# Optimization experiments

Measured on AMD Instinct MI355X. Metric: run time of the kernel, lower is better.

## Reference

```python
import jax, jax.numpy as jnp
import numpy as np

N = 8192      # nodes
E = 262144    # edges (avg degree 32)
D_IN = 128    # feat dim (out_channels)
D_H = 256     # hidden_channels * 2
D_OUT = 64    # in_channels (final embedding dim)


def _sage_pool(feat, src, dst, n, Wp, bp, Ws, Wn, b, ew):
    # DGL SAGEConv('pool'): h_pool = relu(fc_pool(feat)); msg = h_pool[src] * ew;
    # h_neigh = max over in-edges (0 for isolated nodes);
    # out = fc_self(feat) + fc_neigh(h_neigh) + bias
    h = jax.nn.relu(feat @ Wp + bp)                          # [N, d_in]
    msg = h[src] * ew[:, None]                               # [E, d_in]
    agg = jax.ops.segment_max(msg, dst, num_segments=n)      # [N, d_in], -inf if no in-edges
    agg = jnp.where(jnp.isfinite(agg), agg, 0.0)
    return feat @ Ws + agg @ Wn + b


def setup_inputs() -> dict:
    key = jax.random.key(0)
    ks = jax.random.split(key, 20)
    feat = jax.random.normal(ks[0], (N, D_IN), dtype=jnp.float32)
    src = jax.random.randint(ks[1], (E,), 0, N)
    dst = jax.random.randint(ks[2], (E,), 0, N)
    edge_weight = jax.random.uniform(ks[3], (E,), dtype=jnp.float32)

    def lin(k, din, dout):
        return jax.random.normal(k, (din, dout), dtype=jnp.float32) / np.float32(np.sqrt(din))

    params = {}
    dims = [(D_IN, D_H), (D_H, D_H), (D_H, D_OUT)]
    i = 4
    for l, (di, do) in enumerate(dims, 1):
        params[f"Wp{l}"] = lin(ks[i], di, di); i += 1
        params[f"bp{l}"] = jnp.zeros((di,), jnp.float32)
        params[f"Ws{l}"] = lin(ks[i], di, do); i += 1
        params[f"Wn{l}"] = lin(ks[i], di, do); i += 1
        params[f"b{l}"] = jnp.zeros((do,), jnp.float32)

    return dict(feat=feat, src=src, dst=dst, edge_weight=edge_weight, n_nodes=N, **params)


def reference(feat, src, dst, edge_weight, n_nodes,
              Wp1, bp1, Ws1, Wn1, b1,
              Wp2, bp2, Ws2, Wn2, b2,
              Wp3, bp3, Ws3, Wn3, b3):
    hd = jax.nn.relu(_sage_pool(feat, src, dst, n_nodes, Wp1, bp1, Ws1, Wn1, b1, edge_weight))
    hd = jax.nn.relu(_sage_pool(hd,   src, dst, n_nodes, Wp2, bp2, Ws2, Wn2, b2, edge_weight))
    hd = jax.nn.relu(_sage_pool(hd,   src, dst, n_nodes, Wp3, bp3, Ws3, Wn3, b3, edge_weight))
    adj_rec = hd @ hd.T                                      # [N, N]
    return hd, adj_rec
```

## Files before the change

### kernel.cpp

```cpp
#include <hip/hip_runtime.h>
#include <hip/hip_bf16.h>

#define NN 8192
#define NE 262144
#define CAP 96

typedef __attribute__((ext_vector_type(8))) __bf16 bf16x8;
typedef __attribute__((ext_vector_type(4))) float f32x4;

__device__ __forceinline__ ushort f2b(float v) {
    __hip_bfloat16 b = __float2bfloat16(v);
    return *reinterpret_cast<ushort*>(&b);
}
__device__ __forceinline__ uint pack2(float lo, float hi) {
    return (uint)f2b(lo) | ((uint)f2b(hi) << 16);
}
__device__ __forceinline__ float b2f(ushort u) {
    return __uint_as_float(((uint)u) << 16);
}

struct PrepArgs {
    const int* src; const int* dst; const float* ew;
    int* cnt; uint2* slots;
    const float* w[9]; ushort* wt[9];
};

__global__ __launch_bounds__(256) void prep_scatter_k(PrepArgs a) {
    const int bid = blockIdx.x, tid = threadIdx.x;
    if (bid < 1024) {
        int e = bid * 256 + tid;
        int d = a.dst[e];
        int p = atomicAdd(&a.cnt[d], 1);
        if (p < CAP) a.slots[(size_t)d * CAP + p] = make_uint2((uint)a.src[e], __float_as_uint(a.ew[e]));
        return;
    }
    int id = (bid - 1024) * 256 + tid;
    if (id >= 376832) return;
    const int cum[10] = {0, 16384, 49152, 81920, 147456, 212992, 278528, 344064, 360448, 376832};
    const int KK[9] = {128, 128, 128, 256, 256, 256, 256, 256, 256};
    const int LN[9] = {7, 8, 8, 8, 8, 8, 8, 6, 6};
    int m = 0;
#pragma unroll
    for (int t = 1; t < 9; ++t) m += (id >= cum[t]);
    int local = id - cum[m];
    int K = KK[m], ln = LN[m];
    int k = local >> ln, n = local & ((1 << ln) - 1);
    a.wt[m][n * K + k] = f2b(a.w[m][local]);
}

#define AWK 136

template <int BM, int BN, bool A1F32, bool RELU, int OUTMODE, bool ADDC>
__global__ __launch_bounds__(256, 4) void gemm_k(
    const void* __restrict__ Av, const ushort* __restrict__ BT, int K,
    const float* __restrict__ bias, const ushort* __restrict__ cin,
    float* __restrict__ Cf, ushort* __restrict__ Cb, int N) {
    constexpr int MI = BM / 32, NJ = BN / 32;
    __shared__ __align__(16) ushort As[BM * AWK];
    __shared__ __align__(16) ushort Bs[BN * AWK];

    const int tid = threadIdx.x, lane = tid & 63, wave = tid >> 6;
    const int wm = (wave >> 1) * (BM / 2), wn = (wave & 1) * (BN / 2);
    const int r16 = lane & 15, kb = lane >> 4;
    const int m0 = blockIdx.y * BM, n0 = blockIdx.x * BN;

    f32x4 acc[MI][NJ];
#pragma unroll
    for (int i = 0; i < MI; ++i)
#pragma unroll
        for (int j = 0; j < NJ; ++j) acc[i][j] = (f32x4)(0.f);

    for (int k0 = 0; k0 < K; k0 += 128) {
        if constexpr (A1F32) {
            const float* A = (const float*)Av;
#pragma unroll
            for (int rep = 0; rep < BM / 8; ++rep) {
                int id = rep * 256 + tid;
                int row = id >> 5, c = id & 31;
                float4 f = *(const float4*)&A[(size_t)(m0 + row) * K + k0 + c * 4];
                uint2 o; o.x = pack2(f.x, f.y); o.y = pack2(f.z, f.w);
                *(uint2*)&As[row * AWK + c * 4] = o;
            }
        } else {
            const ushort* A = (const ushort*)Av;
#pragma unroll
            for (int rep = 0; rep < BM / 16; ++rep) {
                int id = rep * 256 + tid;
                int row = id >> 4, c = id & 15;
                *(bf16x8*)&As[row * AWK + c * 8] =
                    *(const bf16x8*)&A[(size_t)(m0 + row) * K + k0 + c * 8];
            }
        }
#pragma unroll
        for (int rep = 0; rep < BN / 16; ++rep) {
            int id = rep * 256 + tid;
            int row = id >> 4, c = id & 15;
            *(bf16x8*)&Bs[row * AWK + c * 8] =
                *(const bf16x8*)&BT[(size_t)(n0 + row) * K + k0 + c * 8];
        }
        __syncthreads();
#pragma unroll
        for (int kc = 0; kc < 4; ++kc) {
            bf16x8 a[MI], b[NJ];
#pragma unroll
            for (int i = 0; i < MI; ++i)
                a[i] = *(const bf16x8*)&As[(wm + 16 * i + r16) * AWK + kc * 32 + kb * 8];
#pragma unroll
            for (int j = 0; j < NJ; ++j)
                b[j] = *(const bf16x8*)&Bs[(wn + 16 * j + r16) * AWK + kc * 32 + kb * 8];
#pragma unroll
            for (int i = 0; i < MI; ++i)
#pragma unroll
                for (int j = 0; j < NJ; ++j)
                    acc[i][j] = __builtin_amdgcn_mfma_f32_16x16x32_bf16(a[i], b[j], acc[i][j], 0, 0, 0);
        }
        __syncthreads();
    }

#pragma unroll
    for (int i = 0; i < MI; ++i) {
#pragma unroll
        for (int j = 0; j < NJ; ++j) {
            int col = n0 + wn + 16 * j + r16;
            float bv = ADDC ? 0.f : bias[col];
#pragma unroll
            for (int r = 0; r < 4; ++r) {
                int row = m0 + wm + 16 * i + kb * 4 + r;
                float v = acc[i][j][r];
                if constexpr (ADDC) v += b2f(cin[(size_t)row * N + col]);
                else v += bv;
                if (RELU) v = fmaxf(v, 0.f);
                if (OUTMODE != 0) Cf[(size_t)row * N + col] = v;
                if (OUTMODE != 1) Cb[(size_t)row * N + col] = f2b(v);
            }
        }
    }
}

template <int DIN, int DOUT, bool A1F32>
__global__ __launch_bounds__(256, 4) void seg_self_k(
    const ushort* __restrict__ Pin, const int* __restrict__ cnt,
    const uint2* __restrict__ slots, ushort* __restrict__ G,
    const void* __restrict__ Av, const ushort* __restrict__ WsT,
    const float* __restrict__ bias, ushort* __restrict__ Cself) {
    constexpr int BM = (DOUT == 64) ? 32 : 64;
    constexpr int NBX = DOUT / 64;
    constexpr int MI = BM / 32, NJ = 2;
    __shared__ __align__(16) ushort As[BM * AWK];
    __shared__ __align__(16) ushort Bs[64 * AWK];

    const int tid = threadIdx.x, lane = tid & 63, wave = tid >> 6;

    if (blockIdx.x < 2048) {
        constexpr int FPL = DIN / 64;
        int node = blockIdx.x * 4 + wave;
        int f0 = lane * FPL;
        int n = cnt[node]; if (n > CAP) n = CAP;
        const uint2* sl = &slots[(size_t)node * CAP];
        float mx[FPL];
#pragma unroll
        for (int i = 0; i < FPL; ++i) mx[i] = 0.f;
        auto upd = [&](uint s, float w) {
            const uint* hp = (const uint*)&Pin[(size_t)s * DIN + f0];
#pragma unroll
            for (int c = 0; c < FPL / 2; ++c) {
                uint u = hp[c];
                float lo = __uint_as_float(u << 16);
                float hi = __uint_as_float(u & 0xffff0000u);
                mx[2 * c] = fmaxf(mx[2 * c], lo * w);
                mx[2 * c + 1] = fmaxf(mx[2 * c + 1], hi * w);
            }
        };
        int e = 0;
        for (; e + 8 <= n; e += 8) {
            uint2 d[8];
#pragma unroll
            for (int t = 0; t < 8; ++t) d[t] = sl[e + t];
#pragma unroll
            for (int t = 0; t < 8; ++t) upd(d[t].x, __uint_as_float(d[t].y));
        }
        for (; e < n; ++e) { uint2 d = sl[e]; upd(d.x, __uint_as_float(d.y)); }
        uint* gp = (uint*)&G[(size_t)node * DIN + f0];
#pragma unroll
        for (int c = 0; c < FPL / 2; ++c) gp[c] = pack2(mx[2 * c], mx[2 * c + 1]);
        return;
    }

    const int bx = blockIdx.x - 2048;
    const int n0 = (bx % NBX) * 64, m0 = (bx / NBX) * BM;
    const int wm = (wave >> 1) * (BM / 2), wn = (wave & 1) * 32;
    const int r16 = lane & 15, kb = lane >> 4;

    f32x4 acc[MI][NJ];
#pragma unroll
    for (int i = 0; i < MI; ++i)
#pragma unroll
        for (int j = 0; j < NJ; ++j) acc[i][j] = (f32x4)(0.f);

    for (int k0 = 0; k0 < DIN; k0 += 128) {
        if constexpr (A1F32) {
            const float* A = (const float*)Av;
#pragma unroll
            for (int rep = 0; rep < BM / 8; ++rep) {
                int id = rep * 256 + tid;
                int row = id >> 5, c = id & 31;
                float4 f = *(const float4*)&A[(size_t)(m0 + row) * DIN + k0 + c * 4];
                uint2 o; o.x = pack2(f.x, f.y); o.y = pack2(f.z, f.w);
                *(uint2*)&As[row * AWK + c * 4] = o;
            }
        } else {
            const ushort* A = (const ushort*)Av;
#pragma unroll
            for (int rep = 0; rep < BM / 16; ++rep) {
                int id = rep * 256 + tid;
                int row = id >> 4, c = id & 15;
                *(bf16x8*)&As[row * AWK + c * 8] =
                    *(const bf16x8*)&A[(size_t)(m0 + row) * DIN + k0 + c * 8];
            }
        }
#pragma unroll
        for (int rep = 0; rep < 4; ++rep) {
            int id = rep * 256 + tid;
            int row = id >> 4, c = id & 15;
            *(bf16x8*)&Bs[row * AWK + c * 8] =
                *(const bf16x8*)&WsT[(size_t)(n0 + row) * DIN + k0 + c * 8];
        }
        __syncthreads();
#pragma unroll
        for (int kc = 0; kc < 4; ++kc) {
            bf16x8 a[MI], b[NJ];
#pragma unroll
            for (int i = 0; i < MI; ++i)
                a[i] = *(const bf16x8*)&As[(wm + 16 * i + r16) * AWK + kc * 32 + kb * 8];
#pragma unroll
            for (int j = 0; j < NJ; ++j)
                b[j] = *(const bf16x8*)&Bs[(wn + 16 * j + r16) * AWK + kc * 32 + kb * 8];
#pragma unroll
            for (int i = 0; i < MI; ++i)
#pragma unroll
                for (int j = 0; j < NJ; ++j)
                    acc[i][j] = __builtin_amdgcn_mfma_f32_16x16x32_bf16(a[i], b[j], acc[i][j], 0, 0, 0);
        }
        __syncthreads();
    }

#pragma unroll
    for (int i = 0; i < MI; ++i) {
#pragma unroll
        for (int j = 0; j < NJ; ++j) {
            int col = n0 + wn + 16 * j + r16;
            float bv = bias[col];
#pragma unroll
            for (int r = 0; r < 4; ++r) {
                int row = m0 + wm + 16 * i + kb * 4 + r;
                Cself[(size_t)row * DOUT + col] = f2b(acc[i][j][r] + bv);
            }
        }
    }
}

__global__ __launch_bounds__(256) void aat_k(const ushort* __restrict__ H,
                                             float* __restrict__ C) {
    __shared__ __align__(16) ushort As[128 * 72];
    __shared__ __align__(16) ushort Bs[128 * 72];
    int tid = threadIdx.x, lane = tid & 63, wave = tid >> 6;
    int wm = (wave >> 1) * 64, wn = (wave & 1) * 64;
    int r16 = lane & 15, kb = lane >> 4;
    int m0 = blockIdx.y * 128, n0 = blockIdx.x * 128;

#pragma unroll
    for (int rep = 0; rep < 4; ++rep) {
        int id = rep * 256 + tid;
        int row = id >> 3, c = id & 7;
        *(bf16x8*)&As[row * 72 + c * 8] = *(const bf16x8*)&H[(size_t)(m0 + row) * 64 + c * 8];
        *(bf16x8*)&Bs[row * 72 + c * 8] = *(const bf16x8*)&H[(size_t)(n0 + row) * 64 + c * 8];
    }
    __syncthreads();

    f32x4 acc[4][4];
#pragma unroll
    for (int i = 0; i < 4; ++i)
#pragma unroll
        for (int j = 0; j < 4; ++j) acc[i][j] = (f32x4)(0.f);

#pragma unroll
    for (int kc = 0; kc < 2; ++kc) {
        bf16x8 a[4], b[4];
#pragma unroll
        for (int i = 0; i < 4; ++i)
            a[i] = *(const bf16x8*)&As[(wm + 16 * i + r16) * 72 + kc * 32 + kb * 8];
#pragma unroll
        for (int j = 0; j < 4; ++j)
            b[j] = *(const bf16x8*)&Bs[(wn + 16 * j + r16) * 72 + kc * 32 + kb * 8];
#pragma unroll
        for (int i = 0; i < 4; ++i)
#pragma unroll
            for (int j = 0; j < 4; ++j)
                acc[i][j] = __builtin_amdgcn_mfma_f32_16x16x32_bf16(a[i], b[j], acc[i][j], 0, 0, 0);
    }

#pragma unroll
    for (int i = 0; i < 4; ++i) {
#pragma unroll
        for (int j = 0; j < 4; ++j) {
            int col = n0 + wn + 16 * j + r16;
#pragma unroll
            for (int r = 0; r < 4; ++r) {
                size_t row = m0 + wm + 16 * i + kb * 4 + r;
                C[row * NN + col] = acc[i][j][r];
            }
        }
    }
}

extern "C" void kernel_launch(void* const* d_in, const int* in_sizes, int n_in,
                              void* d_out, int out_size, void* d_ws, size_t ws_size,
                              hipStream_t stream) {
    const float* feat = (const float*)d_in[0];
    const int* src = (const int*)d_in[1];
    const int* dst = (const int*)d_in[2];
    const float* ew = (const float*)d_in[3];
    const float* Wp1 = (const float*)d_in[5];
    const float* bp1 = (const float*)d_in[6];
    const float* Ws1 = (const float*)d_in[7];
    const float* Wn1 = (const float*)d_in[8];
    const float* b1  = (const float*)d_in[9];
    const float* Wp2 = (const float*)d_in[10];
    const float* bp2 = (const float*)d_in[11];
    const float* Ws2 = (const float*)d_in[12];
    const float* Wn2 = (const float*)d_in[13];
    const float* b2  = (const float*)d_in[14];
    const float* Wp3 = (const float*)d_in[15];
    const float* bp3 = (const float*)d_in[16];
    const float* Ws3 = (const float*)d_in[17];
    const float* Wn3 = (const float*)d_in[18];
    const float* b3  = (const float*)d_in[19];

    float* out = (float*)d_out;
    float* adj = out + (size_t)NN * 64;

    char* ws = (char*)d_ws;
    int* cnt      = (int*)(ws + 0x0);
    uint2* slots  = (uint2*)(ws + 0x10000);
    ushort* Wp1T = (ushort*)(ws + 0x620000);
    ushort* Ws1T = (ushort*)(ws + 0x628000);
    ushort* Wn1T = (ushort*)(ws + 0x638000);
    ushort* Wp2T = (ushort*)(ws + 0x648000);
    ushort* Ws2T = (ushort*)(ws + 0x668000);
    ushort* Wn2T = (ushort*)(ws + 0x688000);
    ushort* Wp3T = (ushort*)(ws + 0x6A8000);
    ushort* Ws3T = (ushort*)(ws + 0x6C8000);
    ushort* Wn3T = (ushort*)(ws + 0x6D0000);
    ushort* P  = (ushort*)(ws + 0x700000);
    ushort* G  = (ushort*)(ws + 0xB00000);
    ushort* X  = (ushort*)(ws + 0xF00000);
    ushort* Y  = (ushort*)(ws + 0x1300000);
    ushort* Cs = (ushort*)(ws + 0x1700000);
    ushort* hdb = (ushort*)(ws + 0x1B00000);

    hipMemsetAsync(cnt, 0, NN * sizeof(int), stream);

    PrepArgs pa;
    pa.src = src; pa.dst = dst; pa.ew = ew; pa.cnt = cnt; pa.slots = slots;
    const float* wsrc[9] = {Wp1, Ws1, Wn1, Wp2, Ws2, Wn2, Wp3, Ws3, Wn3};
    ushort* wdst[9] = {Wp1T, Ws1T, Wn1T, Wp2T, Ws2T, Wn2T, Wp3T, Ws3T, Wn3T};
    for (int i = 0; i < 9; ++i) { pa.w[i] = wsrc[i]; pa.wt[i] = wdst[i]; }
    prep_scatter_k<<<1024 + 1472, 256, 0, stream>>>(pa);

    gemm_k<64, 64, true, true, 0, false><<<dim3(2, 128), 256, 0, stream>>>(
        feat, Wp1T, 128, bp1, nullptr, nullptr, P, 128);
    seg_self_k<128, 256, true><<<2048 + 512, 256, 0, stream>>>(
        P, cnt, slots, G, feat, Ws1T, b1, Cs);
    gemm_k<64, 64, false, true, 0, true><<<dim3(4, 128), 256, 0, stream>>>(
        G, Wn1T, 128, nullptr, Cs, nullptr, X, 256);

    gemm_k<64, 64, false, true, 0, false><<<dim3(4, 128), 256, 0, stream>>>(
        X, Wp2T, 256, bp2, nullptr, nullptr, P, 256);
    seg_self_k<256, 256, false><<<2048 + 512, 256, 0, stream>>>(
        P, cnt, slots, G, X, Ws2T, b2, Cs);
    gemm_k<64, 64, false, true, 0, true><<<dim3(4, 128), 256, 0, stream>>>(
        G, Wn2T, 256, nullptr, Cs, nullptr, Y, 256);

    gemm_k<64, 64, false, true, 0, false><<<dim3(4, 128), 256, 0, stream>>>(
        Y, Wp3T, 256, bp3, nullptr, nullptr, P, 256);
    seg_self_k<256, 64, false><<<2048 + 256, 256, 0, stream>>>(
        P, cnt, slots, G, Y, Ws3T, b3, Cs);
    gemm_k<32, 64, false, true, 2, true><<<dim3(1, 256), 256, 0, stream>>>(
        G, Wn3T, 256, nullptr, Cs, out, hdb, 64);

    aat_k<<<dim3(NN / 128, NN / 128), 256, 0, stream>>>(hdb, adj);
}
```

Before: 165.3 us.

## Fuse pool and self projections into one GEMM, split segment-max kernel

Measured after the change: 187.1 us. +13.2%, slower.

```diff
diff --git a/kernel.cpp b/kernel.cpp
--- a/kernel.cpp
+++ b/kernel.cpp
@@ -4,6 +4,7 @@
 #define NN 8192
 #define NE 262144
 #define CAP 96
+#define AWK 136
 
 typedef __attribute__((ext_vector_type(8))) __bf16 bf16x8;
 typedef __attribute__((ext_vector_type(4))) float f32x4;
@@ -23,6 +24,9 @@
     const int* src; const int* dst; const float* ew;
     int* cnt; uint2* slots;
     const float* w[9]; ushort* wt[9];
+    const float* bp1; const float* b1; const float* bp2; const float* b2;
+    const float* bp3; const float* b3;
+    float* bcat1; float* bcat2; float* bcat3;
 };
 
 __global__ __launch_bounds__(256) void prep_scatter_k(PrepArgs a) {
@@ -34,6 +38,17 @@
         if (p < CAP) a.slots[(size_t)d * CAP + p] = make_uint2((uint)a.src[e], __float_as_uint(a.ew[e]));
         return;
     }
+    if (bid == 2496) {
+        for (int i = tid; i < 128; i += 256) a.bcat1[i] = a.bp1[i];
+        for (int i = tid; i < 256; i += 256) {
+            a.bcat1[128 + i] = a.b1[i];
+            a.bcat2[i] = a.bp2[i];
+            a.bcat2[256 + i] = a.b2[i];
+            a.bcat3[i] = a.bp3[i];
+        }
+        for (int i = tid; i < 64; i += 256) a.bcat3[256 + i] = a.b3[i];
+        return;
+    }
     int id = (bid - 1024) * 256 + tid;
     if (id >= 376832) return;
     const int cum[10] = {0, 16384, 49152, 81920, 147456, 212992, 278528, 344064, 360448, 376832};
@@ -48,33 +63,29 @@
     a.wt[m][n * K + k] = f2b(a.w[m][local]);
 }
 
-#define AWK 136
-
-template <int BM, int BN, bool A1F32, bool RELU, int OUTMODE, bool ADDC>
-__global__ __launch_bounds__(256, 4) void gemm_k(
-    const void* __restrict__ Av, const ushort* __restrict__ BT, int K,
-    const float* __restrict__ bias, const ushort* __restrict__ cin,
-    float* __restrict__ Cf, ushort* __restrict__ Cb, int N) {
-    constexpr int MI = BM / 32, NJ = BN / 32;
-    __shared__ __align__(16) ushort As[BM * AWK];
-    __shared__ __align__(16) ushort Bs[BN * AWK];
+template <int NP, int NS, bool A1F32>
+__global__ __launch_bounds__(256, 4) void ps_gemm_k(
+    const void* __restrict__ Av, const ushort* __restrict__ WT, int K,
+    const float* __restrict__ bcat, ushort* __restrict__ P, ushort* __restrict__ Cs) {
+    __shared__ __align__(16) ushort As[64 * AWK];
+    __shared__ __align__(16) ushort Bs[64 * AWK];
 
     const int tid = threadIdx.x, lane = tid & 63, wave = tid >> 6;
-    const int wm = (wave >> 1) * (BM / 2), wn = (wave & 1) * (BN / 2);
+    const int wm = (wave >> 1) * 32, wn = (wave & 1) * 32;
     const int r16 = lane & 15, kb = lane >> 4;
-    const int m0 = blockIdx.y * BM, n0 = blockIdx.x * BN;
-
-    f32x4 acc[MI][NJ];
-#pragma unroll
-    for (int i = 0; i < MI; ++i)
-#pragma unroll
-        for (int j = 0; j < NJ; ++j) acc[i][j] = (f32x4)(0.f);
+    const int m0 = blockIdx.y * 64, n0 = blockIdx.x * 64;
+
+    f32x4 acc[2][2];
+#pragma unroll
+    for (int i = 0; i < 2; ++i)
+#pragma unroll
+        for (int j = 0; j < 2; ++j) acc[i][j] = (f32x4)(0.f);
 
     for (int k0 = 0; k0 < K; k0 += 128) {
         if constexpr (A1F32) {
             const float* A = (const float*)Av;
 #pragma unroll
-            for (int rep = 0; rep < BM / 8; ++rep) {
+            for (int rep = 0; rep < 8; ++rep) {
                 int id = rep * 256 + tid;
                 int row = id >> 5, c = id & 31;
                 float4 f = *(const float4*)&A[(size_t)(m0 + row) * K + k0 + c * 4];
@@ -84,7 +95,7 @@
         } else {
             const ushort* A = (const ushort*)Av;
 #pragma unroll
-            for (int rep = 0; rep < BM / 16; ++rep) {
+            for (int rep = 0; rep < 4; ++rep) {
                 int id = rep * 256 + tid;
                 int row = id >> 4, c = id & 15;
                 *(bf16x8*)&As[row * AWK + c * 8] =
@@ -92,153 +103,101 @@
             }
         }
 #pragma unroll
-        for (int rep = 0; rep < BN / 16; ++rep) {
-            int id = rep * 256 + tid;
-            int row = id >> 4, c = id & 15;
-            *(bf16x8*)&Bs[row * AWK + c * 8] =
-                *(const bf16x8*)&BT[(size_t)(n0 + row) * K + k0 + c * 8];
-        }
-        __syncthreads();
-#pragma unroll
-        for (int kc = 0; kc < 4; ++kc) {
-            bf16x8 a[MI], b[NJ];
-#pragma unroll
-            for (int i = 0; i < MI; ++i)
-                a[i] = *(const bf16x8*)&As[(wm + 16 * i + r16) * AWK + kc * 32 + kb * 8];
-#pragma unroll
-            for (int j = 0; j < NJ; ++j)
-                b[j] = *(const bf16x8*)&Bs[(wn + 16 * j + r16) * AWK + kc * 32 + kb * 8];
-#pragma unroll
-            for (int i = 0; i < MI; ++i)
-#pragma unroll
-                for (int j = 0; j < NJ; ++j)
-                    acc[i][j] = __builtin_amdgcn_mfma_f32_16x16x32_bf16(a[i], b[j], acc[i][j], 0, 0, 0);
-        }
-        __syncthreads();
-    }
-
-#pragma unroll
-    for (int i = 0; i < MI; ++i) {
-#pragma unroll
-        for (int j = 0; j < NJ; ++j) {
-            int col = n0 + wn + 16 * j + r16;
-            float bv = ADDC ? 0.f : bias[col];
-#pragma unroll
-            for (int r = 0; r < 4; ++r) {
-                int row = m0 + wm + 16 * i + kb * 4 + r;
-                float v = acc[i][j][r];
-                if constexpr (ADDC) v += b2f(cin[(size_t)row * N + col]);
-                else v += bv;
-                if (RELU) v = fmaxf(v, 0.f);
-                if (OUTMODE != 0) Cf[(size_t)row * N + col] = v;
-                if (OUTMODE != 1) Cb[(size_t)row * N + col] = f2b(v);
-            }
-        }
-    }
-}
-
-template <int DIN, int DOUT, bool A1F32>
-__global__ __launch_bounds__(256, 4) void seg_self_k(
-    const ushort* __restrict__ Pin, const int* __restrict__ cnt,
-    const uint2* __restrict__ slots, ushort* __restrict__ G,
-    const void* __restrict__ Av, const ushort* __restrict__ WsT,
-    const float* __restrict__ bias, ushort* __restrict__ Cself) {
-    constexpr int BM = (DOUT == 64) ? 32 : 64;
-    constexpr int NBX = DOUT / 64;
-    constexpr int MI = BM / 32, NJ = 2;
-    __shared__ __align__(16) ushort As[BM * AWK];
-    __shared__ __align__(16) ushort Bs[64 * AWK];
-
-    const int tid = threadIdx.x, lane = tid & 63, wave = tid >> 6;
-
-    if (blockIdx.x < 2048) {
-        constexpr int FPL = DIN / 64;
-        int node = blockIdx.x * 4 + wave;
-        int f0 = lane * FPL;
-        int n = cnt[node]; if (n > CAP) n = CAP;
-        const uint2* sl = &slots[(size_t)node * CAP];
-        float mx[FPL];
-#pragma unroll
-        for (int i = 0; i < FPL; ++i) mx[i] = 0.f;
-        auto upd = [&](uint s, float w) {
-            const uint* hp = (const uint*)&Pin[(size_t)s * DIN + f0];
-#pragma unroll
-            for (int c = 0; c < FPL / 2; ++c) {
-                uint u = hp[c];
-                float lo = __uint_as_float(u << 16);
-                float hi = __uint_as_float(u & 0xffff0000u);
-                mx[2 * c] = fmaxf(mx[2 * c], lo * w);
-                mx[2 * c + 1] = fmaxf(mx[2 * c + 1], hi * w);
-            }
-        };
-        int e = 0;
-        for (; e + 8 <= n; e += 8) {
-            uint2 d[8];
-#pragma unroll
-            for (int t = 0; t < 8; ++t) d[t] = sl[e + t];
-#pragma unroll
-            for (int t = 0; t < 8; ++t) upd(d[t].x, __uint_as_float(d[t].y));
-        }
-        for (; e < n; ++e) { uint2 d = sl[e]; upd(d.x, __uint_as_float(d.y)); }
-        uint* gp = (uint*)&G[(size_t)node * DIN + f0];
-#pragma unroll
-        for (int c = 0; c < FPL / 2; ++c) gp[c] = pack2(mx[2 * c], mx[2 * c + 1]);
-        return;
-    }
-
-    const int bx = blockIdx.x - 2048;
-    const int n0 = (bx % NBX) * 64, m0 = (bx / NBX) * BM;
-    const int wm = (wave >> 1) * (BM / 2), wn = (wave & 1) * 32;
-    const int r16 = lane & 15, kb = lane >> 4;
-
-    f32x4 acc[MI][NJ];
-#pragma unroll
-    for (int i = 0; i < MI; ++i)
-#pragma unroll
-        for (int j = 0; j < NJ; ++j) acc[i][j] = (f32x4)(0.f);
-
-    for (int k0 = 0; k0 < DIN; k0 += 128) {
-        if constexpr (A1F32) {
-            const float* A = (const float*)Av;
-#pragma unroll
-            for (int rep = 0; rep < BM / 8; ++rep) {
-                int id = rep * 256 + tid;
-                int row = id >> 5, c = id & 31;
-                float4 f = *(const float4*)&A[(size_t)(m0 + row) * DIN + k0 + c * 4];
-                uint2 o; o.x = pack2(f.x, f.y); o.y = pack2(f.z, f.w);
-                *(uint2*)&As[row * AWK + c * 4] = o;
-            }
-        } else {
-            const ushort* A = (const ushort*)Av;
-#pragma unroll
-            for (int rep = 0; rep < BM / 16; ++rep) {
-                int id = rep * 256 + tid;
-                int row = id >> 4, c = id & 15;
-                *(bf16x8*)&As[row * AWK + c * 8] =
-                    *(const bf16x8*)&A[(size_t)(m0 + row) * DIN + k0 + c * 8];
-            }
-        }
-#pragma unroll
         for (int rep = 0; rep < 4; ++rep) {
             int id = rep * 256 + tid;
             int row = id >> 4, c = id & 15;
             *(bf16x8*)&Bs[row * AWK + c * 8] =
-                *(const bf16x8*)&WsT[(size_t)(n0 + row) * DIN + k0 + c * 8];
+                *(const bf16x8*)&WT[(size_t)(n0 + row) * K + k0 + c * 8];
         }
         __syncthreads();
 #pragma unroll
         for (int kc = 0; kc < 4; ++kc) {
-            bf16x8 a[MI], b[NJ];
+            bf16x8 a[2], b[2];
+#pragma unroll
+            for (int i = 0; i < 2; ++i)
+                a[i] = *(const bf16x8*)&As[(wm + 16 * i + r16) * AWK + kc * 32 + kb * 8];
+#pragma unroll
+            for (int j = 0; j < 2; ++j)
+                b[j] = *(const bf16x8*)&Bs[(wn + 16 * j + r16) * AWK + kc * 32 + kb * 8];
+#pragma unroll
+            for (int i = 0; i < 2; ++i)
+#pragma unroll
+                for (int j = 0; j < 2; ++j)
+                    acc[i][j] = __builtin_amdgcn_mfma_f32_16x16x32_bf16(a[i], b[j], acc[i][j], 0, 0, 0);
+        }
+        __syncthreads();
+    }
+
+    const bool toP = (n0 < NP);
+    ushort* Co = toP ? P : Cs;
+    const int Nout = toP ? NP : NS;
+    const int nb = toP ? n0 : (n0 - NP);
+#pragma unroll
+    for (int i = 0; i < 2; ++i) {
+#pragma unroll
+        for (int j = 0; j < 2; ++j) {
+            int cl = wn + 16 * j + r16;
+            float bv = bcat[n0 + cl];
+#pragma unroll
+            for (int r = 0; r < 4; ++r) {
+                int row = m0 + wm + 16 * i + kb * 4 + r;
+                float v = acc[i][j][r] + bv;
+                if (toP) v = fmaxf(v, 0.f);
+                Co[(size_t)row * Nout + nb + cl] = f2b(v);
+            }
+        }
+    }
+}
+
+template <int BM, bool OUTF>
+__global__ __launch_bounds__(256, 4) void neigh_gemm_k(
+    const ushort* __restrict__ G, const ushort* __restrict__ WnT, int K,
+    const ushort* __restrict__ Cs, float* __restrict__ Cf,
+    ushort* __restrict__ Cb, int N) {
+    constexpr int MI = BM / 32;
+    __shared__ __align__(16) ushort As[BM * AWK];
+    __shared__ __align__(16) ushort Bs[64 * AWK];
+
+    const int tid = threadIdx.x, lane = tid & 63, wave = tid >> 6;
+    const int wm = (wave >> 1) * (BM / 2), wn = (wave & 1) * 32;
+    const int r16 = lane & 15, kb = lane >> 4;
+    const int m0 = blockIdx.y * BM, n0 = blockIdx.x * 64;
+
+    f32x4 acc[MI][2];
+#pragma unroll
+    for (int i = 0; i < MI; ++i)
+#pragma unroll
+        for (int j = 0; j < 2; ++j) acc[i][j] = (f32x4)(0.f);
+
+    for (int k0 = 0; k0 < K; k0 += 128) {
+#pragma unroll
+        for (int rep = 0; rep < BM / 16; ++rep) {
+            int id = rep * 256 + tid;
+            int row = id >> 4, c = id & 15;
+            *(bf16x8*)&As[row * AWK + c * 8] =
+                *(const bf16x8*)&G[(size_t)(m0 + row) * K + k0 + c * 8];
+        }
+#pragma unroll
+        for (int rep = 0; rep < 4; ++rep) {
+            int id = rep * 256 + tid;
+            int row = id >> 4, c = id & 15;
+            *(bf16x8*)&Bs[row * AWK + c * 8] =
+                *(const bf16x8*)&WnT[(size_t)(n0 + row) * K + k0 + c * 8];
+        }
+        __syncthreads();
+#pragma unroll
+        for (int kc = 0; kc < 4; ++kc) {
+            bf16x8 a[MI], b[2];
 #pragma unroll
             for (int i = 0; i < MI; ++i)
                 a[i] = *(const bf16x8*)&As[(wm + 16 * i + r16) * AWK + kc * 32 + kb * 8];
 #pragma unroll
-            for (int j = 0; j < NJ; ++j)
+            for (int j = 0; j < 2; ++j)
                 b[j] = *(const bf16x8*)&Bs[(wn + 16 * j + r16) * AWK + kc * 32 + kb * 8];
 #pragma unroll
             for (int i = 0; i < MI; ++i)
 #pragma unroll
-                for (int j = 0; j < NJ; ++j)
+                for (int j = 0; j < 2; ++j)
                     acc[i][j] = __builtin_amdgcn_mfma_f32_16x16x32_bf16(a[i], b[j], acc[i][j], 0, 0, 0);
         }
         __syncthreads();
@@ -247,16 +206,56 @@
 #pragma unroll
     for (int i = 0; i < MI; ++i) {
 #pragma unroll
-        for (int j = 0; j < NJ; ++j) {
+        for (int j = 0; j < 2; ++j) {
             int col = n0 + wn + 16 * j + r16;
-            float bv = bias[col];
 #pragma unroll
             for (int r = 0; r < 4; ++r) {
                 int row = m0 + wm + 16 * i + kb * 4 + r;
-                Cself[(size_t)row * DOUT + col] = f2b(acc[i][j][r] + bv);
-            }
-        }
-    }
+                float v = acc[i][j][r] + b2f(Cs[(size_t)row * N + col]);
+                v = fmaxf(v, 0.f);
+                if constexpr (OUTF) Cf[(size_t)row * N + col] = v;
+                Cb[(size_t)row * N + col] = f2b(v);
+            }
+        }
+    }
+}
+
+template <int DIN>
+__global__ __launch_bounds__(256) void seg_k(
+    const ushort* __restrict__ Pin, const int* __restrict__ cnt,
+    const uint2* __restrict__ slots, ushort* __restrict__ G) {
+    constexpr int FPL = DIN / 64;
+    const int lane = threadIdx.x & 63, wave = threadIdx.x >> 6;
+    int node = blockIdx.x * 4 + wave;
+    int f0 = lane * FPL;
+    int n = cnt[node]; if (n > CAP) n = CAP;
+    const uint2* sl = &slots[(size_t)node * CAP];
+    float mx[FPL];
+#pragma unroll
+    for (int i = 0; i < FPL; ++i) mx[i] = 0.f;
+    auto upd = [&](uint s, float w) {
+        const uint* hp = (const uint*)&Pin[(size_t)s * DIN + f0];
+#pragma unroll
+        for (int c = 0; c < FPL / 2; ++c) {
+            uint u = hp[c];
+            float lo = __uint_as_float(u << 16);
+            float hi = __uint_as_float(u & 0xffff0000u);
+            mx[2 * c] = fmaxf(mx[2 * c], lo * w);
+            mx[2 * c + 1] = fmaxf(mx[2 * c + 1], hi * w);
+        }
+    };
+    int e = 0;
+    for (; e + 8 <= n; e += 8) {
+        uint2 d[8];
+#pragma unroll
+        for (int t = 0; t < 8; ++t) d[t] = sl[e + t];
+#pragma unroll
+        for (int t = 0; t < 8; ++t) upd(d[t].x, __uint_as_float(d[t].y));
+    }
+    for (; e < n; ++e) { uint2 d = sl[e]; upd(d.x, __uint_as_float(d.y)); }
+    uint* gp = (uint*)&G[(size_t)node * DIN + f0];
+#pragma unroll
+    for (int c = 0; c < FPL / 2; ++c) gp[c] = pack2(mx[2 * c], mx[2 * c + 1]);
 }
 
 __global__ __launch_bounds__(256) void aat_k(const ushort* __restrict__ H,
@@ -307,7 +306,7 @@
 #pragma unroll
             for (int r = 0; r < 4; ++r) {
                 size_t row = m0 + wm + 16 * i + kb * 4 + r;
-                C[row * NN + col] = acc[i][j][r];
+                __builtin_nontemporal_store(acc[i][j][r], &C[row * NN + col]);
             }
         }
     }
@@ -342,15 +341,15 @@
     char* ws = (char*)d_ws;
     int* cnt      = (int*)(ws + 0x0);
     uint2* slots  = (uint2*)(ws + 0x10000);
-    ushort* Wp1T = (ushort*)(ws + 0x620000);
-    ushort* Ws1T = (ushort*)(ws + 0x628000);
-    ushort* Wn1T = (ushort*)(ws + 0x638000);
-    ushort* Wp2T = (ushort*)(ws + 0x648000);
-    ushort* Ws2T = (ushort*)(ws + 0x668000);
-    ushort* Wn2T = (ushort*)(ws + 0x688000);
-    ushort* Wp3T = (ushort*)(ws + 0x6A8000);
-    ushort* Ws3T = (ushort*)(ws + 0x6C8000);
-    ushort* Wn3T = (ushort*)(ws + 0x6D0000);
+    ushort* WpsT1 = (ushort*)(ws + 0x620000);
+    ushort* WpsT2 = (ushort*)(ws + 0x638000);
+    ushort* WpsT3 = (ushort*)(ws + 0x678000);
+    ushort* WnT1  = (ushort*)(ws + 0x6A0000);
+    ushort* WnT2  = (ushort*)(ws + 0x6B0000);
+    ushort* WnT3  = (ushort*)(ws + 0x6D0000);
+    float* bcat1  = (float*)(ws + 0x6D8000);
+    float* bcat2  = (float*)(ws + 0x6D9000);
+    float* bcat3  = (float*)(ws + 0x6DB000);
     ushort* P  = (ushort*)(ws + 0x700000);
     ushort* G  = (ushort*)(ws + 0xB00000);
     ushort* X  = (ushort*)(ws + 0xF00000);
@@ -363,30 +362,31 @@
     PrepArgs pa;
     pa.src = src; pa.dst = dst; pa.ew = ew; pa.cnt = cnt; pa.slots = slots;
     const float* wsrc[9] = {Wp1, Ws1, Wn1, Wp2, Ws2, Wn2, Wp3, Ws3, Wn3};
-    ushort* wdst[9] = {Wp1T, Ws1T, Wn1T, Wp2T, Ws2T, Wn2T, Wp3T, Ws3T, Wn3T};
+    ushort* wdst[9] = {WpsT1, WpsT1 + 128 * 128, WnT1,
+                       WpsT2, WpsT2 + 256 * 256, WnT2,
+                       WpsT3, WpsT3 + 256 * 256, WnT3};
     for (int i = 0; i < 9; ++i) { pa.w[i] = wsrc[i]; pa.wt[i] = wdst[i]; }
-    prep_scatter_k<<<1024 + 1472, 256, 0, stream>>>(pa);
-
-    gemm_k<64, 64, true, true, 0, false><<<dim3(2, 128), 256, 0, stream>>>(
-        feat, Wp1T, 128, bp1, nullptr, nullptr, P, 128);
-    seg_self_k<128, 256, true><<<2048 + 512, 256, 0, stream>>>(
-        P, cnt, slots, G, feat, Ws1T, b1, Cs);
-    gemm_k<64, 64, false, true, 0, true><<<dim3(4, 128), 256, 0, stream>>>(
-        G, Wn1T, 128, nullptr, Cs, nullptr, X, 256);
-
-    gemm_k<64, 64, false, true, 0, false><<<dim3(4, 128), 256, 0, stream>>>(
-        X, Wp2T, 256, bp2, nullptr, nullptr, P, 256);
-    seg_self_k<256, 256, false><<<2048 + 512, 256, 0, stream>>>(
-        P, cnt, slots, G, X, Ws2T, b2, Cs);
-    gemm_k<64, 64, false, true, 0, true><<<dim3(4, 128), 256, 0, stream>>>(
-        G, Wn2T, 256, nullptr, Cs, nullptr, Y, 256);
-
-    gemm_k<64, 64, false, true, 0, false><<<dim3(4, 128), 256, 0, stream>>>(
-        Y, Wp3T, 256, bp3, nullptr, nullptr, P, 256);
-    seg_self_k<256, 64, false><<<2048 + 256, 256, 0, stream>>>(
-        P, cnt, slots, G, Y, Ws3T, b3, Cs);
-    gemm_k<32, 64, false, true, 2, true><<<dim3(1, 256), 256, 0, stream>>>(
-        G, Wn3T, 256, nullptr, Cs, out, hdb, 64);
+    pa.bp1 = bp1; pa.b1 = b1; pa.bp2 = bp2; pa.b2 = b2; pa.bp3 = bp3; pa.b3 = b3;
+    pa.bcat1 = bcat1; pa.bcat2 = bcat2; pa.bcat3 = bcat3;
+    prep_scatter_k<<<2497, 256, 0, stream>>>(pa);
+
+    ps_gemm_k<128, 256, true><<<dim3(6, 128), 256, 0, stream>>>(
+        feat, WpsT1, 128, bcat1, P, Cs);
+    seg_k<128><<<NN / 4, 256, 0, stream>>>(P, cnt, slots, G);
+    neigh_gemm_k<64, false><<<dim3(4, 128), 256, 0, stream>>>(
+        G, WnT1, 128, Cs, nullptr, X, 256);
+
+    ps_gemm_k<256, 256, false><<<dim3(8, 128), 256, 0, stream>>>(
+        X, WpsT2, 256, bcat2, P, Cs);
+    seg_k<256><<<NN / 4, 256, 0, stream>>>(P, cnt, slots, G);
+    neigh_gemm_k<64, false><<<dim3(4, 128), 256, 0, stream>>>(
+        G, WnT2, 256, Cs, nullptr, Y, 256);
+
+    ps_gemm_k<256, 64, false><<<dim3(5, 128), 256, 0, stream>>>(
+        Y, WpsT3, 256, bcat3, P, Cs);
+    seg_k<256><<<NN / 4, 256, 0, stream>>>(P, cnt, slots, G);
+    neigh_gemm_k<32, true><<<dim3(1, 256), 256, 0, stream>>>(
+        G, WnT3, 256, Cs, out, hdb, 64);
 
     aat_k<<<dim3(NN / 128, NN / 128), 256, 0, stream>>>(hdb, adj);
 }
```

## Fuse edge scatter with layer-1 pool GEMM and interleave segment/GEMM blocks

Applied to the files above, without the earlier changes.

After: 163.0 us, median of 2. No clear change (-1.4%).

```diff
diff --git a/kernel.cpp b/kernel.cpp
--- a/kernel.cpp
+++ b/kernel.cpp
@@ -4,6 +4,7 @@
 #define NN 8192
 #define NE 262144
 #define CAP 96
+#define AWK 136
 
 typedef __attribute__((ext_vector_type(8))) __bf16 bf16x8;
 typedef __attribute__((ext_vector_type(4))) float f32x4;
@@ -19,62 +20,28 @@
     return __uint_as_float(((uint)u) << 16);
 }
 
-struct PrepArgs {
-    const int* src; const int* dst; const float* ew;
-    int* cnt; uint2* slots;
-    const float* w[9]; ushort* wt[9];
-};
-
-__global__ __launch_bounds__(256) void prep_scatter_k(PrepArgs a) {
-    const int bid = blockIdx.x, tid = threadIdx.x;
-    if (bid < 1024) {
-        int e = bid * 256 + tid;
-        int d = a.dst[e];
-        int p = atomicAdd(&a.cnt[d], 1);
-        if (p < CAP) a.slots[(size_t)d * CAP + p] = make_uint2((uint)a.src[e], __float_as_uint(a.ew[e]));
-        return;
-    }
-    int id = (bid - 1024) * 256 + tid;
-    if (id >= 376832) return;
-    const int cum[10] = {0, 16384, 49152, 81920, 147456, 212992, 278528, 344064, 360448, 376832};
-    const int KK[9] = {128, 128, 128, 256, 256, 256, 256, 256, 256};
-    const int LN[9] = {7, 8, 8, 8, 8, 8, 8, 6, 6};
-    int m = 0;
-#pragma unroll
-    for (int t = 1; t < 9; ++t) m += (id >= cum[t]);
-    int local = id - cum[m];
-    int K = KK[m], ln = LN[m];
-    int k = local >> ln, n = local & ((1 << ln) - 1);
-    a.wt[m][n * K + k] = f2b(a.w[m][local]);
-}
-
-#define AWK 136
-
-template <int BM, int BN, bool A1F32, bool RELU, int OUTMODE, bool ADDC>
-__global__ __launch_bounds__(256, 4) void gemm_k(
-    const void* __restrict__ Av, const ushort* __restrict__ BT, int K,
-    const float* __restrict__ bias, const ushort* __restrict__ cin,
-    float* __restrict__ Cf, ushort* __restrict__ Cb, int N) {
-    constexpr int MI = BM / 32, NJ = BN / 32;
-    __shared__ __align__(16) ushort As[BM * AWK];
-    __shared__ __align__(16) ushort Bs[BN * AWK];
-
+template <bool A1F32, bool RELU, int OUTMODE, bool ADDC>
+__device__ __forceinline__ void gemm_tile64(
+    int by, int bx, const void* __restrict__ Av, const ushort* __restrict__ BT,
+    int K, const float* __restrict__ bias, const ushort* __restrict__ cin,
+    float* __restrict__ Cf, ushort* __restrict__ Cb, int N,
+    ushort* As, ushort* Bs) {
     const int tid = threadIdx.x, lane = tid & 63, wave = tid >> 6;
-    const int wm = (wave >> 1) * (BM / 2), wn = (wave & 1) * (BN / 2);
+    const int wm = (wave >> 1) * 32, wn = (wave & 1) * 32;
     const int r16 = lane & 15, kb = lane >> 4;
-    const int m0 = blockIdx.y * BM, n0 = blockIdx.x * BN;
-
-    f32x4 acc[MI][NJ];
-#pragma unroll
-    for (int i = 0; i < MI; ++i)
-#pragma unroll
-        for (int j = 0; j < NJ; ++j) acc[i][j] = (f32x4)(0.f);
+    const int m0 = by * 64, n0 = bx * 64;
+
+    f32x4 acc[2][2];
+#pragma unroll
+    for (int i = 0; i < 2; ++i)
+#pragma unroll
+        for (int j = 0; j < 2; ++j) acc[i][j] = (f32x4)(0.f);
 
     for (int k0 = 0; k0 < K; k0 += 128) {
         if constexpr (A1F32) {
             const float* A = (const float*)Av;
 #pragma unroll
-            for (int rep = 0; rep < BM / 8; ++rep) {
+            for (int rep = 0; rep < 8; ++rep) {
                 int id = rep * 256 + tid;
                 int row = id >> 5, c = id & 31;
                 float4 f = *(const float4*)&A[(size_t)(m0 + row) * K + k0 + c * 4];
@@ -84,7 +51,7 @@
         } else {
             const ushort* A = (const ushort*)Av;
 #pragma unroll
-            for (int rep = 0; rep < BM / 16; ++rep) {
+            for (int rep = 0; rep < 4; ++rep) {
                 int id = rep * 256 + tid;
                 int row = id >> 4, c = id & 15;
                 *(bf16x8*)&As[row * AWK + c * 8] =
@@ -92,7 +59,7 @@
             }
         }
 #pragma unroll
-        for (int rep = 0; rep < BN / 16; ++rep) {
+        for (int rep = 0; rep < 4; ++rep) {
             int id = rep * 256 + tid;
             int row = id >> 4, c = id & 15;
             *(bf16x8*)&Bs[row * AWK + c * 8] =
@@ -101,26 +68,26 @@
         __syncthreads();
 #pragma unroll
         for (int kc = 0; kc < 4; ++kc) {
-            bf16x8 a[MI], b[NJ];
-#pragma unroll
-            for (int i = 0; i < MI; ++i)
+            bf16x8 a[2], b[2];
+#pragma unroll
+            for (int i = 0; i < 2; ++i)
                 a[i] = *(const bf16x8*)&As[(wm + 16 * i + r16) * AWK + kc * 32 + kb * 8];
 #pragma unroll
-            for (int j = 0; j < NJ; ++j)
+            for (int j = 0; j < 2; ++j)
                 b[j] = *(const bf16x8*)&Bs[(wn + 16 * j + r16) * AWK + kc * 32 + kb * 8];
 #pragma unroll
-            for (int i = 0; i < MI; ++i)
-#pragma unroll
-                for (int j = 0; j < NJ; ++j)
+            for (int i = 0; i < 2; ++i)
+#pragma unroll
+                for (int j = 0; j < 2; ++j)
                     acc[i][j] = __builtin_amdgcn_mfma_f32_16x16x32_bf16(a[i], b[j], acc[i][j], 0, 0, 0);
         }
         __syncthreads();
     }
 
 #pragma unroll
-    for (int i = 0; i < MI; ++i) {
-#pragma unroll
-        for (int j = 0; j < NJ; ++j) {
+    for (int i = 0; i < 2; ++i) {
+#pragma unroll
+        for (int j = 0; j < 2; ++j) {
             int col = n0 + wn + 16 * j + r16;
             float bv = ADDC ? 0.f : bias[col];
 #pragma unroll
@@ -137,126 +104,112 @@
     }
 }
 
-template <int DIN, int DOUT, bool A1F32>
+template <int DIN>
+__device__ __forceinline__ void seg4(
+    int grp, const ushort* __restrict__ Pin, const int* __restrict__ cnt,
+    const uint2* __restrict__ slots, ushort* __restrict__ G) {
+    constexpr int FPL = DIN / 64;
+    const int lane = threadIdx.x & 63, wave = threadIdx.x >> 6;
+    int node = grp * 4 + wave;
+    int f0 = lane * FPL;
+    int n = cnt[node]; if (n > CAP) n = CAP;
+    const uint2* sl = &slots[(size_t)node * CAP];
+    float mx[FPL];
+#pragma unroll
+    for (int i = 0; i < FPL; ++i) mx[i] = 0.f;
+    auto upd = [&](uint s, float w) {
+        const uint* hp = (const uint*)&Pin[(size_t)s * DIN + f0];
+#pragma unroll
+        for (int c = 0; c < FPL / 2; ++c) {
+            uint u = hp[c];
+            float lo = __uint_as_float(u << 16);
+            float hi = __uint_as_float(u & 0xffff0000u);
+            mx[2 * c] = fmaxf(mx[2 * c], lo * w);
+            mx[2 * c + 1] = fmaxf(mx[2 * c + 1], hi * w);
+        }
+    };
+    int e = 0;
+    for (; e + 8 <= n; e += 8) {
+        uint2 d[8];
+#pragma unroll
+        for (int t = 0; t < 8; ++t) d[t] = sl[e + t];
+#pragma unroll
+        for (int t = 0; t < 8; ++t) upd(d[t].x, __uint_as_float(d[t].y));
+    }
+    for (; e < n; ++e) { uint2 d = sl[e]; upd(d.x, __uint_as_float(d.y)); }
+    uint* gp = (uint*)&G[(size_t)node * DIN + f0];
+#pragma unroll
+    for (int c = 0; c < FPL / 2; ++c) gp[c] = pack2(mx[2 * c], mx[2 * c + 1]);
+}
+
+struct PrepArgs {
+    int* cnt;
+    const float* w[9]; ushort* wt[9];
+};
+
+__global__ __launch_bounds__(256) void prep_k(PrepArgs a) {
+    const int bid = blockIdx.x, tid = threadIdx.x;
+    if (bid < 32) { a.cnt[bid * 256 + tid] = 0; return; }
+    int id = (bid - 32) * 256 + tid;
+    if (id >= 376832) return;
+    const int cum[10] = {0, 16384, 49152, 81920, 147456, 212992, 278528, 344064, 360448, 376832};
+    const int KK[9] = {128, 128, 128, 256, 256, 256, 256, 256, 256};
+    const int LN[9] = {7, 8, 8, 8, 8, 8, 8, 6, 6};
+    int m = 0;
+#pragma unroll
+    for (int t = 1; t < 9; ++t) m += (id >= cum[t]);
+    int local = id - cum[m];
+    int K = KK[m], ln = LN[m];
+    int k = local >> ln, n = local & ((1 << ln) - 1);
+    a.wt[m][n * K + k] = f2b(a.w[m][local]);
+}
+
+__global__ __launch_bounds__(256, 4) void scat_pool1_k(
+    const int* __restrict__ src, const int* __restrict__ dst,
+    const float* __restrict__ ew, int* __restrict__ cnt, uint2* __restrict__ slots,
+    const float* __restrict__ feat, const ushort* __restrict__ WpT,
+    const float* __restrict__ bp, ushort* __restrict__ P) {
+    __shared__ __align__(16) ushort As[64 * AWK];
+    __shared__ __align__(16) ushort Bs[64 * AWK];
+    const int g = blockIdx.x / 5, r = blockIdx.x % 5;
+    if (r == 4) {
+        gemm_tile64<true, true, 0, false>(g >> 1, g & 1, feat, WpT, 128,
+                                          bp, nullptr, nullptr, P, 128, As, Bs);
+    } else {
+        int e = (g * 4 + r) * 256 + threadIdx.x;
+        int d = dst[e];
+        int p = atomicAdd(&cnt[d], 1);
+        if (p < CAP) slots[(size_t)d * CAP + p] = make_uint2((uint)src[e], __float_as_uint(ew[e]));
+    }
+}
+
+template <int DIN, int RATIO, bool A1F32, int KSELF, int NSELF>
 __global__ __launch_bounds__(256, 4) void seg_self_k(
     const ushort* __restrict__ Pin, const int* __restrict__ cnt,
     const uint2* __restrict__ slots, ushort* __restrict__ G,
     const void* __restrict__ Av, const ushort* __restrict__ WsT,
-    const float* __restrict__ bias, ushort* __restrict__ Cself) {
-    constexpr int BM = (DOUT == 64) ? 32 : 64;
-    constexpr int NBX = DOUT / 64;
-    constexpr int MI = BM / 32, NJ = 2;
-    __shared__ __align__(16) ushort As[BM * AWK];
+    const float* __restrict__ bias, ushort* __restrict__ Cs) {
+    __shared__ __align__(16) ushort As[64 * AWK];
     __shared__ __align__(16) ushort Bs[64 * AWK];
-
-    const int tid = threadIdx.x, lane = tid & 63, wave = tid >> 6;
-
-    if (blockIdx.x < 2048) {
-        constexpr int FPL = DIN / 64;
-        int node = blockIdx.x * 4 + wave;
-        int f0 = lane * FPL;
-        int n = cnt[node]; if (n > CAP) n = CAP;
-        const uint2* sl = &slots[(size_t)node * CAP];
-        float mx[FPL];
-#pragma unroll
-        for (int i = 0; i < FPL; ++i) mx[i] = 0.f;
-        auto upd = [&](uint s, float w) {
-            const uint* hp = (const uint*)&Pin[(size_t)s * DIN + f0];
-#pragma unroll
-            for (int c = 0; c < FPL / 2; ++c) {
-                uint u = hp[c];
-                float lo = __uint_as_float(u << 16);
-                float hi = __uint_as_float(u & 0xffff0000u);
-                mx[2 * c] = fmaxf(mx[2 * c], lo * w);
-                mx[2 * c + 1] = fmaxf(mx[2 * c + 1], hi * w);
-            }
-        };
-        int e = 0;
-        for (; e + 8 <= n; e += 8) {
-            uint2 d[8];
-#pragma unroll
-            for (int t = 0; t < 8; ++t) d[t] = sl[e + t];
-#pragma unroll
-            for (int t = 0; t < 8; ++t) upd(d[t].x, __uint_as_float(d[t].y));
-        }
-        for (; e < n; ++e) { uint2 d = sl[e]; upd(d.x, __uint_as_float(d.y)); }
-        uint* gp = (uint*)&G[(size_t)node * DIN + f0];
-#pragma unroll
-        for (int c = 0; c < FPL / 2; ++c) gp[c] = pack2(mx[2 * c], mx[2 * c + 1]);
-        return;
-    }
-
-    const int bx = blockIdx.x - 2048;
-    const int n0 = (bx % NBX) * 64, m0 = (bx / NBX) * BM;
-    const int wm = (wave >> 1) * (BM / 2), wn = (wave & 1) * 32;
-    const int r16 = lane & 15, kb = lane >> 4;
-
-    f32x4 acc[MI][NJ];
-#pragma unroll
-    for (int i = 0; i < MI; ++i)
-#pragma unroll
-        for (int j = 0; j < NJ; ++j) acc[i][j] = (f32x4)(0.f);
-
-    for (int k0 = 0; k0 < DIN; k0 += 128) {
-        if constexpr (A1F32) {
-            const float* A = (const float*)Av;
-#pragma unroll
-            for (int rep = 0; rep < BM / 8; ++rep) {
-                int id = rep * 256 + tid;
-                int row = id >> 5, c = id & 31;
-                float4 f = *(const float4*)&A[(size_t)(m0 + row) * DIN + k0 + c * 4];
-                uint2 o; o.x = pack2(f.x, f.y); o.y = pack2(f.z, f.w);
-                *(uint2*)&As[row * AWK + c * 4] = o;
-            }
-        } else {
-            const ushort* A = (const ushort*)Av;
-#pragma unroll
-            for (int rep = 0; rep < BM / 16; ++rep) {
-                int id = rep * 256 + tid;
-                int row = id >> 4, c = id & 15;
-                *(bf16x8*)&As[row * AWK + c * 8] =
-                    *(const bf16x8*)&A[(size_t)(m0 + row) * DIN + k0 + c * 8];
-            }
-        }
-#pragma unroll
-        for (int rep = 0; rep < 4; ++rep) {
-            int id = rep * 256 + tid;
-            int row = id >> 4, c = id & 15;
-            *(bf16x8*)&Bs[row * AWK + c * 8] =
-                *(const bf16x8*)&WsT[(size_t)(n0 + row) * DIN + k0 + c * 8];
-        }
-        __syncthreads();
-#pragma unroll
-        for (int kc = 0; kc < 4; ++kc) {
-            bf16x8 a[MI], b[NJ];
-#pragma unroll
-            for (int i = 0; i < MI; ++i)
-                a[i] = *(const bf16x8*)&As[(wm + 16 * i + r16) * AWK + kc * 32 + kb * 8];
-#pragma unroll
-            for (int j = 0; j < NJ; ++j)
-                b[j] = *(const bf16x8*)&Bs[(wn + 16 * j + r16) * AWK + kc * 32 + kb * 8];
-#pragma unroll
-            for (int i = 0; i < MI; ++i)
-#pragma unroll
-                for (int j = 0; j < NJ; ++j)
-                    acc[i][j] = __builtin_amdgcn_mfma_f32_16x16x32_bf16(a[i], b[j], acc[i][j], 0, 0, 0);
-        }
-        __syncthreads();
-    }
-
-#pragma unroll
-    for (int i = 0; i < MI; ++i) {
-#pragma unroll
-        for (int j = 0; j < NJ; ++j) {
-            int col = n0 + wn + 16 * j + r16;
-            float bv = bias[col];
-#pragma unroll
-            for (int r = 0; r < 4; ++r) {
-                int row = m0 + wm + 16 * i + kb * 4 + r;
-                Cself[(size_t)row * DOUT + col] = f2b(acc[i][j][r] + bv);
-            }
-        }
-    }
+    const int g = blockIdx.x / (RATIO + 1), r = blockIdx.x % (RATIO + 1);
+    if (r == RATIO) {
+        constexpr int NBX = NSELF / 64;
+        gemm_tile64<A1F32, false, 0, false>(g / NBX, g % NBX, Av, WsT, KSELF,
+                                            bias, nullptr, nullptr, Cs, NSELF, As, Bs);
+    } else {
+        seg4<DIN>(g * RATIO + r, Pin, cnt, slots, G);
+    }
+}
+
+template <bool A1F32, bool RELU, int OUTMODE, bool ADDC>
+__global__ __launch_bounds__(256, 4) void gemm_k(
+    const void* __restrict__ Av, const ushort* __restrict__ BT, int K,
+    const float* __restrict__ bias, const ushort* __restrict__ cin,
+    float* __restrict__ Cf, ushort* __restrict__ Cb, int N) {
+    __shared__ __align__(16) ushort As[64 * AWK];
+    __shared__ __align__(16) ushort Bs[64 * AWK];
+    gemm_tile64<A1F32, RELU, OUTMODE, ADDC>(blockIdx.y, blockIdx.x, Av, BT, K,
+                                            bias, cin, Cf, Cb, N, As, Bs);
 }
 
 __global__ __launch_bounds__(256) void aat_k(const ushort* __restrict__ H,
@@ -358,34 +311,32 @@
     ushort* Cs = (ushort*)(ws + 0x1700000);
     ushort* hdb = (ushort*)(ws + 0x1B00000);
 
-    hipMemsetAsync(cnt, 0, NN * sizeof(int), stream);
-
     PrepArgs pa;
-    pa.src = src; pa.dst = dst; pa.ew = ew; pa.cnt = cnt; pa.slots = slots;
+    pa.cnt = cnt;
     const float* wsrc[9] = {Wp1, Ws1, Wn1, Wp2, Ws2, Wn2, Wp3, Ws3, Wn3};
     ushort* wdst[9] = {Wp1T, Ws1T, Wn1T, Wp2T, Ws2T, Wn2T, Wp3T, Ws3T, Wn3T};
     for (int i = 0; i < 9; ++i) { pa.w[i] = wsrc[i]; pa.wt[i] = wdst[i]; }
-    prep_scatter_k<<<1024 + 1472, 256, 0, stream>>>(pa);
-
-    gemm_k<64, 64, true, true, 0, false><<<dim3(2, 128), 256, 0, stream>>>(
-        feat, Wp1T, 128, bp1, nullptr, nullptr, P, 128);
-    seg_self_k<128, 256, true><<<2048 + 512, 256, 0, stream>>>(
+    prep_k<<<32 + 1472, 256, 0, stream>>>(pa);
+
+    scat_pool1_k<<<1280, 256, 0, stream>>>(src, dst, ew, cnt, slots, feat, Wp1T, bp1, P);
+
+    seg_self_k<128, 4, true, 128, 256><<<2560, 256, 0, stream>>>(
         P, cnt, slots, G, feat, Ws1T, b1, Cs);
-    gemm_k<64, 64, false, true, 0, true><<<dim3(4, 128), 256, 0, stream>>>(
+    gemm_k<false, true, 0, true><<<dim3(4, 128), 256, 0, stream>>>(
         G, Wn1T, 128, nullptr, Cs, nullptr, X, 256);
 
-    gemm_k<64, 64, false, true, 0, false><<<dim3(4, 128), 256, 0, stream>>>(
+    gemm_k<false, true, 0, false><<<dim3(4, 128), 256, 0, stream>>>(
         X, Wp2T, 256, bp2, nullptr, nullptr, P, 256);
-    seg_self_k<256, 256, false><<<2048 + 512, 256, 0, stream>>>(
+    seg_self_k<256, 4, false, 256, 256><<<2560, 256, 0, stream>>>(
         P, cnt, slots, G, X, Ws2T, b2, Cs);
-    gemm_k<64, 64, false, true, 0, true><<<dim3(4, 128), 256, 0, stream>>>(
+    gemm_k<false, true, 0, true><<<dim3(4, 128), 256, 0, stream>>>(
         G, Wn2T, 256, nullptr, Cs, nullptr, Y, 256);
 
-    gemm_k<64, 64, false, true, 0, false><<<dim3(4, 128), 256, 0, stream>>>(
+    gemm_k<false, true, 0, false><<<dim3(4, 128), 256, 0, stream>>>(
         Y, Wp3T, 256, bp3, nullptr, nullptr, P, 256);
-    seg_self_k<256, 64, false><<<2048 + 256, 256, 0, stream>>>(
+    seg_self_k<256, 16, false, 256, 64><<<2176, 256, 0, stream>>>(
         P, cnt, slots, G, Y, Ws3T, b3, Cs);
-    gemm_k<32, 64, false, true, 2, true><<<dim3(1, 256), 256, 0, stream>>>(
+    gemm_k<false, true, 2, true><<<dim3(1, 128), 256, 0, stream>>>(
         G, Wn3T, 256, nullptr, Cs, out, hdb, 64);
 
     aat_k<<<dim3(NN / 128, NN / 128), 256, 0, stream>>>(hdb, adj);
```
